# Optimization experiments

Hardware: AMD Instinct MI355X
Metric: run time of the kernel (lower is better)

Reference implementation:

```python
import jax, jax.numpy as jnp
from jax import lax
import numpy as np

WINDOW = 8
ENCOLEN = 128
HID = 128
INT_H = 128


def setup_inputs() -> dict:
    key = jax.random.key(0)
    ks = jax.random.split(key, 16)
    s = 0.05
    B, T = 512, 256
    return {
        "input_X": jax.random.normal(ks[0], (B, T, 7), jnp.float32),
        "W_ih": jax.random.normal(ks[1], (4 * HID, 5), jnp.float32) * s,
        "W_hh": jax.random.normal(ks[2], (4 * HID, HID), jnp.float32) * s,
        "b_ih": jax.random.normal(ks[3], (4 * HID,), jnp.float32) * s,
        "b_hh": jax.random.normal(ks[4], (4 * HID,), jnp.float32) * s,
        "fc1_w": jax.random.normal(ks[5], (HID, HID), jnp.float32) * s,
        "fc1_b": jax.random.normal(ks[6], (HID,), jnp.float32) * s,
        "fc2_w": jax.random.normal(ks[7], (1, HID), jnp.float32) * s,
        "fc2_b": jax.random.normal(ks[8], (1,), jnp.float32) * s,
        "int1_w": jax.random.normal(ks[9], (INT_H, 3), jnp.float32) * s,
        "int1_b": jax.random.normal(ks[10], (INT_H,), jnp.float32) * s,
        "int3_w": jax.random.normal(ks[11], (1, INT_H), jnp.float32) * s,
        "int3_b": jax.random.normal(ks[12], (1,), jnp.float32) * s,
        "scale_w": jax.random.normal(ks[13], (1, 1), jnp.float32) * s,
        "zone_w": jax.random.normal(ks[14], (1, 1), jnp.float32) * s,
    }


def _forward(input_X, W_ih, W_hh, b_ih, b_hh, fc1_w, fc1_b, fc2_w, fc2_b,
             int1_w, int1_b, int3_w, int3_b, scale_w, zone_w):
    B, T, _ = input_X.shape
    w = WINDOW
    T0 = input_X[:, :, 0:1]      # zone temperature
    Ext_X = input_X[:, :, 1:5]   # cols [1,2,3,4]
    Int_X = input_X[:, :, 3:6]   # cols [3,4,5]
    HVAC_X = input_X[:, :, 6:7]  # col [6]

    def lstm_chunk(h, c, xs):  # xs: [B, w, 5]
        def step(carry, x_t):
            h, c = carry
            g = x_t @ W_ih.T + b_ih + h @ W_hh.T + b_hh
            gi, gf, gg, go = jnp.split(g, 4, axis=-1)  # torch gate order i,f,g,o
            c = jax.nn.sigmoid(gf) * c + jax.nn.sigmoid(gi) * jnp.tanh(gg)
            h = jax.nn.sigmoid(go) * jnp.tanh(c)
            return (h, c), None
        (h, c), _ = lax.scan(step, (h, c), jnp.swapaxes(xs, 0, 1))
        return h, c  # final h == lstm_out[:, -1, :]

    def ext_module(h, c, xs):
        h, c = lstm_chunk(h, c, xs)
        o = jax.nn.relu(h @ fc1_w.T + fc1_b)
        return o @ fc2_w.T + fc2_b, h, c  # [B,1]

    # internal module is pointwise per timestep -> vectorize over all T
    # (note: FC2 in the torch module is defined but unused; faithful skip)
    int_all = jax.nn.sigmoid(
        jax.nn.relu(Int_X @ int1_w.T + int1_b) @ int3_w.T + int3_b
    ) @ scale_w.T  # [B,T,1]

    TOut = jnp.zeros((B, T, 1), input_X.dtype).at[:, :w].set(T0[:, :w])
    h = jnp.ones((B, HID), input_X.dtype)
    c = jnp.ones((B, HID), input_X.dtype)
    E = T0[:, w:w + 1, :]  # [B,1,1]

    def enc_step(carry, i):
        TOut, h, c, E = carry
        ratio = i.astype(input_X.dtype) / ENCOLEN
        TOut = lax.dynamic_update_slice(TOut, E, (0, i, 0))
        s = i - w + 1
        Tin = lax.dynamic_slice(T0, (0, s, 0), (B, w, 1))
        TOsl = lax.dynamic_slice(TOut, (0, s, 0), (B, w, 1))
        Exsl = lax.dynamic_slice(Ext_X, (0, s, 0), (B, w, 4))
        embed = jnp.concatenate([Tin * ratio + TOsl * (1.0 - ratio), Exsl], axis=2)
        ext, h, c = ext_module(h, c, embed)
        hv = lax.dynamic_slice(HVAC_X, (0, i, 0), (B, 1, 1))[:, 0]
        it = lax.dynamic_slice(int_all, (0, i, 0), (B, 1, 1))[:, 0]
        total = ext + hv + it  # [B,1]
        T0i = lax.dynamic_slice(T0, (0, i, 0), (B, 1, 1))
        E = ratio * T0i + (1.0 - ratio) * E + (total @ zone_w.T)[:, None, :]
        return (TOut, h, c, E), ext

    (TOut, h, c, E), ext_enc = lax.scan(enc_step, (TOut, h, c, E), jnp.arange(w, ENCOLEN))

    def dec_step(carry, i):
        TOut, h, c, E = carry
        TOut = lax.dynamic_update_slice(TOut, E, (0, i, 0))
        s = i - w + 1
        TOsl = lax.dynamic_slice(TOut, (0, s, 0), (B, w, 1))
        Exsl = lax.dynamic_slice(Ext_X, (0, s, 0), (B, w, 4))
        embed = jnp.concatenate([TOsl, Exsl], axis=2)
        ext, h, c = ext_module(h, c, embed)
        hv = lax.dynamic_slice(HVAC_X, (0, i, 0), (B, 1, 1))[:, 0]
        it = lax.dynamic_slice(int_all, (0, i, 0), (B, 1, 1))[:, 0]
        total = ext + hv + it
        E = (total @ zone_w.T)[:, None, :] + E
        return (TOut, h, c, E), ext

    (TOut, h, c, E), ext_dec = lax.scan(dec_step, (TOut, h, c, E), jnp.arange(ENCOLEN, T))

    Ext_list = jnp.zeros((B, T, 1), input_X.dtype)
    Ext_list = Ext_list.at[:, w:ENCOLEN].set(jnp.swapaxes(ext_enc, 0, 1))
    Ext_list = Ext_list.at[:, ENCOLEN:].set(jnp.swapaxes(ext_dec, 0, 1))
    Int_list = jnp.zeros((B, T, 1), input_X.dtype).at[:, w:].set(int_all[:, w:])
    HVAC_list = HVAC_X  # torch fills HVAC_list with HVAC_X at every step
    return TOut, HVAC_list, (Ext_list, Int_list)


def reference(input_X, W_ih, W_hh, b_ih, b_hh, fc1_w, fc1_b, fc2_w, fc2_b,
              int1_w, int1_b, int3_w, int3_b, scale_w, zone_w):
    return _forward(input_X, W_ih, W_hh, b_ih, b_hh, fc1_w, fc1_b, fc2_w, fc2_b,
                    int1_w, int1_b, int3_w, int3_b, scale_w, zone_w)
```

## Files before the change

kernel.cpp:

```cpp
#include <hip/hip_runtime.h>

#define BT   (512*256)
#define HB0  128
#define HB1  288
#define HLEN 448

using short8  = __attribute__((ext_vector_type(8))) short;
using floatx4 = __attribute__((ext_vector_type(4))) float;

__device__ inline unsigned short f2bf(float f){
  unsigned int u = __float_as_uint(f);
  u += 0x7FFFu + ((u >> 16) & 1u);
  return (unsigned short)(u >> 16);
}
__device__ inline float rcpf(float x){ return __builtin_amdgcn_rcpf(x); }

__global__ __launch_bounds__(256,1) void k_seq(
    const float* __restrict__ in,
    const float* __restrict__ Wih,  const float* __restrict__ Whh,
    const float* __restrict__ bih,  const float* __restrict__ bhh,
    const float* __restrict__ fc1w, const float* __restrict__ fc1b,
    const float* __restrict__ fc2w, const float* __restrict__ fc2b,
    const float* __restrict__ i1w,  const float* __restrict__ i1b,
    const float* __restrict__ i3w,  const float* __restrict__ i3b,
    const float* __restrict__ scw,  const float* __restrict__ zonew,
    float* __restrict__ out)
{
  __shared__ __align__(16) unsigned short hbuf[2][HLEN];
  __shared__ float xg[8192];
  __shared__ float obuf[256];
  __shared__ float toutl[512];
  __shared__ float inl[3584];
  __shared__ float itl[512];
  __shared__ float E_l[2], hvit[2], t0i[2];

  const int tid=threadIdx.x, wv=tid>>6, ln=tid&63, l15=ln&15, quad=ln>>4;
  const int bb=blockIdx.x;

  for(int p=tid;p<3584;p+=256) inl[p]=in[bb*3584+p];
  for(int p=tid;p<2*HLEN;p+=256) ((unsigned short*)hbuf)[p]=0;
  __syncthreads();
  hbuf[0][HB0 + (tid>>7)*(HB1-HB0) + (tid&127)] = 0x3F80;
  if(tid<16) toutl[(tid>>3)*256+(tid&7)] = inl[(tid>>3)*1792+(tid&7)*7];
  if(tid<2)  E_l[tid] = inl[tid*1792+56];

  {
    float* lw4 = xg;
    float* l3  = xg + 512;
    if(tid<128){
      lw4[tid*4+0]=i1w[tid*3+0]; lw4[tid*4+1]=i1w[tid*3+1];
      lw4[tid*4+2]=i1w[tid*3+2]; lw4[tid*4+3]=i1b[tid];
      l3[tid]=i3w[tid];
    }
    __syncthreads();
    const float b30=i3b[0], sc0=scw[0];
    #pragma unroll
    for(int rep=0;rep<2;rep++){
      int idx=tid+256*rep, b=idx>>8, t=idx&255;
      const float* row = inl + b*1792 + t*7;
      float x0=row[3],x1=row[4],x2=row[5], acc=0.f;
      #pragma unroll 8
      for(int j=0;j<128;j++){
        float r=fmaxf(lw4[j*4]*x0+lw4[j*4+1]*x1+lw4[j*4+2]*x2+lw4[j*4+3],0.f);
        acc += r*l3[j];
      }
      float v = rcpf(1.f+__expf(-(acc+b30)))*sc0;
      float itv = (t<8)?0.f:v;
      int gb = 2*bb+b;
      itl[b*256+t]=itv;
      out[3*BT+gb*256+t]=itv;
      out[BT+gb*256+t]=row[6];
      if(t<8){ out[gb*256+t]=row[0]; out[2*BT+gb*256+t]=0.f; }
    }
  }

  short8 wfr[4][2][4];
  short8 xfr[4][2];
  short8 ffr[2][4];
  float  bsum[4][2];
  #pragma unroll
  for(int g=0;g<4;g++){
    #pragma unroll
    for(int hh=0;hh<2;hh++){
      int n = 128*g + 32*wv + 16*hh + l15;
      bsum[g][hh] = bih[n]+bhh[n];
      #pragma unroll
      for(int Q=0;Q<4;Q++){
        short8 f;
        #pragma unroll
        for(int j=0;j<8;j++) f[j]=(short)f2bf(Whh[n*128 + Q*32 + quad*8 + j]);
        wfr[g][hh][Q]=f;
      }
      short8 f;
      #pragma unroll
      for(int j=0;j<8;j++){ int kk=quad*8+j; f[j]=(short)f2bf(kk<5?Wih[n*5+kk]:0.f); }
      xfr[g][hh]=f;
    }
  }
  #pragma unroll
  for(int hh=0;hh<2;hh++){
    int n = 32*wv + 16*hh + l15;
    #pragma unroll
    for(int Q=0;Q<4;Q++){
      short8 f;
      #pragma unroll
      for(int j=0;j<8;j++) f[j]=(short)f2bf(fc1w[n*128 + Q*32 + quad*8 + j]);
      ffr[hh][Q]=f;
    }
  }

  const int  u     = 32*wv + 16*(quad>>1) + l15;
  const int  bm    = quad & 1;
  const bool hi2   = quad >= 2;
  const int  aoff  = ((l15&3)==0) ? (HB0 + ((l15>>2)&1)*(HB1-HB0) + quad*8)
                                  : (quad*8);
  const int  xbase = bm*512 + u;
  const int  hwoff = HB0 + bm*(HB1-HB0) + u;
  const float fb    = fc1b[u];
  const float fw0   = fc2w[ln];
  const float fw1   = fc2w[64+ln];
  const float fc2b0 = fc2b[0];
  const float zw    = zonew[0];
  const floatx4 ZV  = {0.f,0.f,0.f,0.f};
  float c0 = 1.f;
  __syncthreads();

  #pragma unroll 1
  for(int i=8;i<256;i++){
    if(tid<2){
      float Ev=E_l[tid];
      toutl[tid*256+i]=Ev;
      out[(2*bb+tid)*256+i]=Ev;
      hvit[tid]=inl[tid*1792+i*7+6]+itl[tid*256+i];
      t0i[tid]=inl[tid*1792+i*7];
    }
    {
      short8 ea = 0;
      if(quad==0){
        int bE=l15>>3, kk=l15&7, p=i-7+kk;
        const float* rp = inl + bE*1792 + p*7;
        float tos = (p==i) ? E_l[bE] : toutl[bE*256+p];
        float tmix;
        if(i<128){
          float ratio=(float)i*0.0078125f;
          tmix = rp[0]*ratio + tos*(1.f-ratio);
        } else tmix = tos;
        ea[0]=(short)f2bf(tmix); ea[1]=(short)f2bf(rp[1]);
        ea[2]=(short)f2bf(rp[2]); ea[3]=(short)f2bf(rp[3]);
        ea[4]=(short)f2bf(rp[4]);
      }
      #pragma unroll
      for(int g=0;g<4;g++){
        #pragma unroll
        for(int hh=0;hh<2;hh++){
          floatx4 z=__builtin_amdgcn_mfma_f32_16x16x32_bf16(ea, xfr[g][hh], ZV,0,0,0);
          #pragma unroll
          for(int r=0;r<4;r++){
            int m=4*quad+r;
            xg[(m&7)*1024 + (m>>3)*512 + 128*g + 32*wv+16*hh+l15] = z[r]+bsum[g][hh];
          }
        }
      }
    }
    __syncthreads();

    #pragma unroll
    for(int k=0;k<8;k++){
      float xv0=xg[k*1024+xbase    ];
      float xv1=xg[k*1024+xbase+128];
      float xv2=xg[k*1024+xbase+256];
      float xv3=xg[k*1024+xbase+384];
      const unsigned short* ab = hbuf[k&1] + aoff;
      short8 a0=*(const short8*)(ab);
      short8 a1=*(const short8*)(ab+32);
      short8 a2=*(const short8*)(ab+64);
      short8 a3=*(const short8*)(ab+96);
      floatx4 acc[4][2];
      #pragma unroll
      for(int g=0;g<4;g++){
        #pragma unroll
        for(int hh=0;hh<2;hh++){
          floatx4 z=__builtin_amdgcn_mfma_f32_16x16x32_bf16(a0,wfr[g][hh][0],ZV,0,0,0);
          z=__builtin_amdgcn_mfma_f32_16x16x32_bf16(a1,wfr[g][hh][1],z,0,0,0);
          z=__builtin_amdgcn_mfma_f32_16x16x32_bf16(a2,wfr[g][hh][2],z,0,0,0);
          z=__builtin_amdgcn_mfma_f32_16x16x32_bf16(a3,wfr[g][hh][3],z,0,0,0);
          acc[g][hh]=z;
        }
      }
      float gi=(hi2?acc[0][1][0]:acc[0][0][0])+xv0;
      float gf=(hi2?acc[1][1][0]:acc[1][0][0])+xv1;
      float gg=(hi2?acc[2][1][0]:acc[2][0][0])+xv2;
      float go=(hi2?acc[3][1][0]:acc[3][0][0])+xv3;
      float ef =__expf(-gf);
      float egi=__expf(-gi);
      float egg=__expf(-2.f*gg);
      float sf = rcpf(1.f+ef);
      float itn=(1.f-egg)*rcpf((1.f+egi)*(1.f+egg));
      c0 = sf*c0 + itn;
      float ego=__expf(-go);
      float ec =__expf(-2.f*c0);
      float hv2=(1.f-ec)*rcpf((1.f+ego)*(1.f+ec));
      hbuf[(k+1)&1][hwoff]=f2bf(hv2);
      __syncthreads();
    }

    {
      const unsigned short* ab = hbuf[0] + aoff;
      short8 a0=*(const short8*)(ab);
      short8 a1=*(const short8*)(ab+32);
      short8 a2=*(const short8*)(ab+64);
      short8 a3=*(const short8*)(ab+96);
      floatx4 fa[2];
      #pragma unroll
      for(int hh=0;hh<2;hh++){
        floatx4 z=__builtin_amdgcn_mfma_f32_16x16x32_bf16(a0,ffr[hh][0],ZV,0,0,0);
        z=__builtin_amdgcn_mfma_f32_16x16x32_bf16(a1,ffr[hh][1],z,0,0,0);
        z=__builtin_amdgcn_mfma_f32_16x16x32_bf16(a2,ffr[hh][2],z,0,0,0);
        z=__builtin_amdgcn_mfma_f32_16x16x32_bf16(a3,ffr[hh][3],z,0,0,0);
        fa[hh]=z;
      }
      float fv = hi2 ? fa[1][0] : fa[0][0];
      obuf[bm*128+u]=fmaxf(fv+fb,0.f);
    }
    __syncthreads();

    if(wv<2){
      float v = obuf[wv*128+ln]*fw0 + obuf[wv*128+64+ln]*fw1;
      #pragma unroll
      for(int off=32; off; off>>=1) v += __shfl_xor(v, off, 64);
      if(ln==0){
        float ext = v + fc2b0;
        float total = ext + hvit[wv];
        float E = E_l[wv];
        if(i<128){
          float ratio=(float)i*0.0078125f;
          E = ratio*t0i[wv] + (1.f-ratio)*E + total*zw;
        } else {
          E = E + total*zw;
        }
        E_l[wv]=E;
        out[2*BT+(2*bb+wv)*256+i]=ext;
      }
    }
    __syncthreads();
  }
}

extern "C" void kernel_launch(void* const* d_in, const int* in_sizes, int n_in,
                              void* d_out, int out_size, void* d_ws, size_t ws_size,
                              hipStream_t stream)
{
  const float* in   = (const float*)d_in[0];
  const float* Wih  = (const float*)d_in[1];
  const float* Whh  = (const float*)d_in[2];
  const float* bih  = (const float*)d_in[3];
  const float* bhh  = (const float*)d_in[4];
  const float* fc1w = (const float*)d_in[5];
  const float* fc1b = (const float*)d_in[6];
  const float* fc2w = (const float*)d_in[7];
  const float* fc2b = (const float*)d_in[8];
  const float* i1w  = (const float*)d_in[9];
  const float* i1b  = (const float*)d_in[10];
  const float* i3w  = (const float*)d_in[11];
  const float* i3b  = (const float*)d_in[12];
  const float* scw  = (const float*)d_in[13];
  const float* zw   = (const float*)d_in[14];
  float* out = (float*)d_out;

  k_seq<<<dim3(256), dim3(256), 0, stream>>>(in, Wih, Whh, bih, bhh,
                                             fc1w, fc1b, fc2w, fc2b,
                                             i1w, i1b, i3w, i3b, scw, zw, out);
}
```

Baseline: 1.181 ms.

## Pack two independent batch groups per block with atomic-counter group barriers

Each 512-thread block now runs two independent 256-thread groups (128 blocks in total), and every __syncthreads is replaced by a per-group LDS atomic counter spin barrier. This lets the two groups' sequential LSTM steps interleave and hide each other's latency. To fit in LDS, the gate pre-activations, TOut and ext history, and ext features are stored as bf16. The ext and TOut outputs are buffered in LDS and written out once at the end. The trade-offs are lower precision for the stored values (TOut is rounded to bf16, which can drift through the recurrence) and spin-wait overhead from the software barriers.

```diff
diff --git a/kernel.cpp b/kernel.cpp
--- a/kernel.cpp
+++ b/kernel.cpp
@@ -4,6 +4,7 @@
 #define HB0  128
 #define HB1  288
 #define HLEN 448
+#define NG   2
 
 using short8  = __attribute__((ext_vector_type(8))) short;
 using floatx4 = __attribute__((ext_vector_type(4))) float;
@@ -13,9 +14,12 @@
   u += 0x7FFFu + ((u >> 16) & 1u);
   return (unsigned short)(u >> 16);
 }
+__device__ inline float bf2f(unsigned short u){
+  return __uint_as_float(((unsigned int)u) << 16);
+}
 __device__ inline float rcpf(float x){ return __builtin_amdgcn_rcpf(x); }
 
-__global__ __launch_bounds__(256,1) void k_seq(
+__global__ __launch_bounds__(512,2) void k_seq(
     const float* __restrict__ in,
     const float* __restrict__ Wih,  const float* __restrict__ Whh,
     const float* __restrict__ bih,  const float* __restrict__ bhh,
@@ -26,38 +30,52 @@
     const float* __restrict__ scw,  const float* __restrict__ zonew,
     float* __restrict__ out)
 {
-  __shared__ __align__(16) unsigned short hbuf[2][HLEN];
-  __shared__ float xg[8192];
-  __shared__ float obuf[256];
-  __shared__ float toutl[512];
-  __shared__ float inl[3584];
-  __shared__ float itl[512];
-  __shared__ float E_l[2], hvit[2], t0i[2];
-
-  const int tid=threadIdx.x, wv=tid>>6, ln=tid&63, l15=ln&15, quad=ln>>4;
-  const int bb=blockIdx.x;
-
-  for(int p=tid;p<3584;p+=256) inl[p]=in[bb*3584+p];
-  for(int p=tid;p<2*HLEN;p+=256) ((unsigned short*)hbuf)[p]=0;
+  __shared__ __align__(16) unsigned short hbuf[NG][2][HLEN];
+  __shared__ __align__(16) unsigned short xgu [NG][8192];
+  __shared__ __align__(8)  unsigned short toutl[NG][512];
+  __shared__ __align__(8)  unsigned short extl [NG][512];
+  __shared__ __align__(8)  unsigned short exl  [NG][2048];
+  __shared__ float t0l  [NG][512];
+  __shared__ float hvitl[NG][512];
+  __shared__ float obuf [NG][256];
+  __shared__ float E_l  [NG][2];
+  __shared__ unsigned int ctr[NG*16];
+
+  const int tid = threadIdx.x;
+  const int g   = tid >> 8;
+  const int t   = tid & 255;
+  const int wv  = t >> 6;
+  const int ln  = t & 63;
+  const int l15 = ln & 15;
+  const int quad= ln >> 4;
+  const int vbb = blockIdx.x*NG + g;
+
+  for(int p=t; p<512; p+=256){
+    int b=p>>8, tt=p&255;
+    const float* row = in + (2*vbb+b)*1792 + tt*7;
+    t0l[g][p] = row[0];
+    exl[g][p*4+0]=f2bf(row[1]); exl[g][p*4+1]=f2bf(row[2]);
+    exl[g][p*4+2]=f2bf(row[3]); exl[g][p*4+3]=f2bf(row[4]);
+  }
+  for(int p=t; p<2*HLEN; p+=256) ((unsigned short*)hbuf[g])[p]=0;
+  hbuf[g][0][HB0 + (t>>7)*(HB1-HB0) + (t&127)] = 0x3F80;
+  if(t<16) toutl[g][(t>>3)*256+(t&7)] = f2bf(in[(2*vbb+(t>>3))*1792+(t&7)*7]);
+  if(t<2)  E_l[g][t] = in[(2*vbb+t)*1792 + 56];
+  if(t==0) ctr[g*16]=0;
+  float* lw4 = (float*)&xgu[g][0];
+  float* l3  = lw4 + 512;
+  if(t<128){
+    lw4[t*4+0]=i1w[t*3+0]; lw4[t*4+1]=i1w[t*3+1];
+    lw4[t*4+2]=i1w[t*3+2]; lw4[t*4+3]=i1b[t];
+    l3[t]=i3w[t];
+  }
   __syncthreads();
-  hbuf[0][HB0 + (tid>>7)*(HB1-HB0) + (tid&127)] = 0x3F80;
-  if(tid<16) toutl[(tid>>3)*256+(tid&7)] = inl[(tid>>3)*1792+(tid&7)*7];
-  if(tid<2)  E_l[tid] = inl[tid*1792+56];
 
   {
-    float* lw4 = xg;
-    float* l3  = xg + 512;
-    if(tid<128){
-      lw4[tid*4+0]=i1w[tid*3+0]; lw4[tid*4+1]=i1w[tid*3+1];
-      lw4[tid*4+2]=i1w[tid*3+2]; lw4[tid*4+3]=i1b[tid];
-      l3[tid]=i3w[tid];
-    }
-    __syncthreads();
     const float b30=i3b[0], sc0=scw[0];
     #pragma unroll
-    for(int rep=0;rep<2;rep++){
-      int idx=tid+256*rep, b=idx>>8, t=idx&255;
-      const float* row = inl + b*1792 + t*7;
+    for(int b=0;b<2;b++){
+      const float* row = in + (2*vbb+b)*1792 + t*7;
       float x0=row[3],x1=row[4],x2=row[5], acc=0.f;
       #pragma unroll 8
       for(int j=0;j<128;j++){
@@ -66,8 +84,8 @@
       }
       float v = rcpf(1.f+__expf(-(acc+b30)))*sc0;
       float itv = (t<8)?0.f:v;
-      int gb = 2*bb+b;
-      itl[b*256+t]=itv;
+      int gb = 2*vbb+b;
+      hvitl[g][b*256+t] = row[6] + itv;
       out[3*BT+gb*256+t]=itv;
       out[BT+gb*256+t]=row[6];
       if(t<8){ out[gb*256+t]=row[0]; out[2*BT+gb*256+t]=0.f; }
@@ -79,22 +97,22 @@
   short8 ffr[2][4];
   float  bsum[4][2];
   #pragma unroll
-  for(int g=0;g<4;g++){
+  for(int gg=0;gg<4;gg++){
     #pragma unroll
     for(int hh=0;hh<2;hh++){
-      int n = 128*g + 32*wv + 16*hh + l15;
-      bsum[g][hh] = bih[n]+bhh[n];
+      int n = 128*gg + 32*wv + 16*hh + l15;
+      bsum[gg][hh] = bih[n]+bhh[n];
       #pragma unroll
       for(int Q=0;Q<4;Q++){
         short8 f;
         #pragma unroll
         for(int j=0;j<8;j++) f[j]=(short)f2bf(Whh[n*128 + Q*32 + quad*8 + j]);
-        wfr[g][hh][Q]=f;
+        wfr[gg][hh][Q]=f;
       }
       short8 f;
       #pragma unroll
       for(int j=0;j<8;j++){ int kk=quad*8+j; f[j]=(short)f2bf(kk<5?Wih[n*5+kk]:0.f); }
-      xfr[g][hh]=f;
+      xfr[gg][hh]=f;
     }
   }
   #pragma unroll
@@ -123,89 +141,92 @@
   const float zw    = zonew[0];
   const floatx4 ZV  = {0.f,0.f,0.f,0.f};
   float c0 = 1.f;
-  __syncthreads();
+
+  unsigned int tgt = 0;
+  volatile unsigned int* vct = (volatile unsigned int*)&ctr[g*16];
+  #define GSYNC() do{ tgt += 4; __threadfence_block();                    \
+      if(ln==0) atomicAdd((unsigned int*)&ctr[g*16], 1u);                 \
+      while(*vct < tgt){}                                                 \
+      __threadfence_block(); }while(0)
+
+  GSYNC();
 
   #pragma unroll 1
   for(int i=8;i<256;i++){
-    if(tid<2){
-      float Ev=E_l[tid];
-      toutl[tid*256+i]=Ev;
-      out[(2*bb+tid)*256+i]=Ev;
-      hvit[tid]=inl[tid*1792+i*7+6]+itl[tid*256+i];
-      t0i[tid]=inl[tid*1792+i*7];
-    }
+    if(t<2) toutl[g][t*256+i] = f2bf(E_l[g][t]);
     {
       short8 ea = 0;
       if(quad==0){
         int bE=l15>>3, kk=l15&7, p=i-7+kk;
-        const float* rp = inl + bE*1792 + p*7;
-        float tos = (p==i) ? E_l[bE] : toutl[bE*256+p];
+        float t0v = t0l[g][bE*256+p];
+        float tos = (p==i) ? E_l[g][bE] : bf2f(toutl[g][bE*256+p]);
         float tmix;
         if(i<128){
           float ratio=(float)i*0.0078125f;
-          tmix = rp[0]*ratio + tos*(1.f-ratio);
+          tmix = t0v*ratio + tos*(1.f-ratio);
         } else tmix = tos;
-        ea[0]=(short)f2bf(tmix); ea[1]=(short)f2bf(rp[1]);
-        ea[2]=(short)f2bf(rp[2]); ea[3]=(short)f2bf(rp[3]);
-        ea[4]=(short)f2bf(rp[4]);
-      }
-      #pragma unroll
-      for(int g=0;g<4;g++){
+        ea[0]=(short)f2bf(tmix);
+        ea[1]=(short)exl[g][(bE*256+p)*4+0]; ea[2]=(short)exl[g][(bE*256+p)*4+1];
+        ea[3]=(short)exl[g][(bE*256+p)*4+2]; ea[4]=(short)exl[g][(bE*256+p)*4+3];
+      }
+      #pragma unroll
+      for(int gg=0;gg<4;gg++){
         #pragma unroll
         for(int hh=0;hh<2;hh++){
-          floatx4 z=__builtin_amdgcn_mfma_f32_16x16x32_bf16(ea, xfr[g][hh], ZV,0,0,0);
+          floatx4 z=__builtin_amdgcn_mfma_f32_16x16x32_bf16(ea, xfr[gg][hh], ZV,0,0,0);
           #pragma unroll
           for(int r=0;r<4;r++){
             int m=4*quad+r;
-            xg[(m&7)*1024 + (m>>3)*512 + 128*g + 32*wv+16*hh+l15] = z[r]+bsum[g][hh];
+            xgu[g][(m&7)*1024 + (m>>3)*512 + 128*gg + 32*wv+16*hh+l15]
+              = f2bf(z[r]+bsum[gg][hh]);
           }
         }
       }
     }
-    __syncthreads();
+    GSYNC();
 
     #pragma unroll
     for(int k=0;k<8;k++){
-      float xv0=xg[k*1024+xbase    ];
-      float xv1=xg[k*1024+xbase+128];
-      float xv2=xg[k*1024+xbase+256];
-      float xv3=xg[k*1024+xbase+384];
-      const unsigned short* ab = hbuf[k&1] + aoff;
+      float xv0=bf2f(xgu[g][k*1024+xbase    ]);
+      float xv1=bf2f(xgu[g][k*1024+xbase+128]);
+      float xv2=bf2f(xgu[g][k*1024+xbase+256]);
+      float xv3=bf2f(xgu[g][k*1024+xbase+384]);
+      const unsigned short* ab = &hbuf[g][k&1][0] + aoff;
       short8 a0=*(const short8*)(ab);
       short8 a1=*(const short8*)(ab+32);
       short8 a2=*(const short8*)(ab+64);
       short8 a3=*(const short8*)(ab+96);
       floatx4 acc[4][2];
       #pragma unroll
-      for(int g=0;g<4;g++){
+      for(int gg=0;gg<4;gg++){
         #pragma unroll
         for(int hh=0;hh<2;hh++){
-          floatx4 z=__builtin_amdgcn_mfma_f32_16x16x32_bf16(a0,wfr[g][hh][0],ZV,0,0,0);
-          z=__builtin_amdgcn_mfma_f32_16x16x32_bf16(a1,wfr[g][hh][1],z,0,0,0);
-          z=__builtin_amdgcn_mfma_f32_16x16x32_bf16(a2,wfr[g][hh][2],z,0,0,0);
-          z=__builtin_amdgcn_mfma_f32_16x16x32_bf16(a3,wfr[g][hh][3],z,0,0,0);
-          acc[g][hh]=z;
+          floatx4 z=__builtin_amdgcn_mfma_f32_16x16x32_bf16(a0,wfr[gg][hh][0],ZV,0,0,0);
+          z=__builtin_amdgcn_mfma_f32_16x16x32_bf16(a1,wfr[gg][hh][1],z,0,0,0);
+          z=__builtin_amdgcn_mfma_f32_16x16x32_bf16(a2,wfr[gg][hh][2],z,0,0,0);
+          z=__builtin_amdgcn_mfma_f32_16x16x32_bf16(a3,wfr[gg][hh][3],z,0,0,0);
+          acc[gg][hh]=z;
         }
       }
       float gi=(hi2?acc[0][1][0]:acc[0][0][0])+xv0;
       float gf=(hi2?acc[1][1][0]:acc[1][0][0])+xv1;
-      float gg=(hi2?acc[2][1][0]:acc[2][0][0])+xv2;
+      float gg2=(hi2?acc[2][1][0]:acc[2][0][0])+xv2;
       float go=(hi2?acc[3][1][0]:acc[3][0][0])+xv3;
       float ef =__expf(-gf);
       float egi=__expf(-gi);
-      float egg=__expf(-2.f*gg);
+      float egg=__expf(-2.f*gg2);
       float sf = rcpf(1.f+ef);
       float itn=(1.f-egg)*rcpf((1.f+egi)*(1.f+egg));
       c0 = sf*c0 + itn;
       float ego=__expf(-go);
       float ec =__expf(-2.f*c0);
       float hv2=(1.f-ec)*rcpf((1.f+ego)*(1.f+ec));
-      hbuf[(k+1)&1][hwoff]=f2bf(hv2);
-      __syncthreads();
+      hbuf[g][(k+1)&1][hwoff]=f2bf(hv2);
+      GSYNC();
     }
 
     {
-      const unsigned short* ab = hbuf[0] + aoff;
+      const unsigned short* ab = &hbuf[g][0][0] + aoff;
       short8 a0=*(const short8*)(ab);
       short8 a1=*(const short8*)(ab+32);
       short8 a2=*(const short8*)(ab+64);
@@ -220,30 +241,39 @@
         fa[hh]=z;
       }
       float fv = hi2 ? fa[1][0] : fa[0][0];
-      obuf[bm*128+u]=fmaxf(fv+fb,0.f);
-    }
-    __syncthreads();
+      obuf[g][bm*128+u]=fmaxf(fv+fb,0.f);
+    }
+    GSYNC();
 
     if(wv<2){
-      float v = obuf[wv*128+ln]*fw0 + obuf[wv*128+64+ln]*fw1;
+      float v = obuf[g][wv*128+ln]*fw0 + obuf[g][wv*128+64+ln]*fw1;
       #pragma unroll
       for(int off=32; off; off>>=1) v += __shfl_xor(v, off, 64);
       if(ln==0){
-        float ext = v + fc2b0;
-        float total = ext + hvit[wv];
-        float E = E_l[wv];
+        float ext   = v + fc2b0;
+        float total = ext + hvitl[g][wv*256+i];
+        float E = E_l[g][wv];
         if(i<128){
           float ratio=(float)i*0.0078125f;
-          E = ratio*t0i[wv] + (1.f-ratio)*E + total*zw;
+          E = ratio*t0l[g][wv*256+i] + (1.f-ratio)*E + total*zw;
         } else {
           E = E + total*zw;
         }
-        E_l[wv]=E;
-        out[2*BT+(2*bb+wv)*256+i]=ext;
-      }
-    }
-    __syncthreads();
-  }
+        E_l[g][wv]=E;
+        extl[g][wv*256+i]=f2bf(ext);
+      }
+    }
+    GSYNC();
+  }
+
+  for(int p=t; p<496; p+=256){
+    int b = (p>=248) ? 1 : 0;
+    int i2 = p - b*248 + 8;
+    int gb = 2*vbb + b;
+    out[gb*256+i2]        = bf2f(toutl[g][b*256+i2]);
+    out[2*BT+gb*256+i2]   = bf2f(extl[g][b*256+i2]);
+  }
+  #undef GSYNC
 }
 
 extern "C" void kernel_launch(void* const* d_in, const int* in_sizes, int n_in,
@@ -267,7 +297,7 @@
   const float* zw   = (const float*)d_in[14];
   float* out = (float*)d_out;
 
-  k_seq<<<dim3(256), dim3(256), 0, stream>>>(in, Wih, Whh, bih, bhh,
+  k_seq<<<dim3(128), dim3(512), 0, stream>>>(in, Wih, Whh, bih, bhh,
                                              fc1w, fc1b, fc2w, fc2b,
                                              i1w, i1b, i3w, i3b, scw, zw, out);
 }
```

Measured after the change: 1.842 ms. +56.0%, slower.

## Double block to 512 threads, halve per-wave MFMA work, bf16 LDS staging

Applied to the files above, without the earlier changes.

Each block now runs 512 threads (8 waves), so each wave owns 16 hidden units instead of 32 and issues half as many MFMA chains per recurrent step. Gate pre-activations, external inputs and output history move to bf16 in LDS. The fc2 reduction is done with per-wave shuffles plus a small partial-sum array, and every thread tracks E redundantly. The T and ext outputs are buffered in LDS and written once at the end. The aim is to shorten the serial per-step critical path, at the cost of heavier barriers across 8 waves and extra rounding error: T is stored as bf16 before output and fed back into the recurrence, and the ext output is also rounded to bf16.

```diff
diff --git a/kernel.cpp b/kernel.cpp
--- a/kernel.cpp
+++ b/kernel.cpp
@@ -13,9 +13,12 @@
   u += 0x7FFFu + ((u >> 16) & 1u);
   return (unsigned short)(u >> 16);
 }
+__device__ inline float bf2f(unsigned short u){
+  return __uint_as_float(((unsigned int)u) << 16);
+}
 __device__ inline float rcpf(float x){ return __builtin_amdgcn_rcpf(x); }
 
-__global__ __launch_bounds__(256,1) void k_seq(
+__global__ __launch_bounds__(512,1) void k_seq(
     const float* __restrict__ in,
     const float* __restrict__ Wih,  const float* __restrict__ Whh,
     const float* __restrict__ bih,  const float* __restrict__ bhh,
@@ -27,138 +30,131 @@
     float* __restrict__ out)
 {
   __shared__ __align__(16) unsigned short hbuf[2][HLEN];
-  __shared__ float xg[8192];
-  __shared__ float obuf[256];
-  __shared__ float toutl[512];
-  __shared__ float inl[3584];
-  __shared__ float itl[512];
-  __shared__ float E_l[2], hvit[2], t0i[2];
-
-  const int tid=threadIdx.x, wv=tid>>6, ln=tid&63, l15=ln&15, quad=ln>>4;
-  const int bb=blockIdx.x;
-
-  for(int p=tid;p<3584;p+=256) inl[p]=in[bb*3584+p];
-  for(int p=tid;p<2*HLEN;p+=256) ((unsigned short*)hbuf)[p]=0;
+  __shared__ __align__(16) unsigned short xg[8192];
+  __shared__ __align__(8)  unsigned short toutl[512];
+  __shared__ __align__(8)  unsigned short extl[512];
+  __shared__ __align__(16) unsigned short exl[2048];
+  __shared__ float t0l[512];
+  __shared__ float hvitl[512];
+  __shared__ float parts[16];
+
+  const int tid = threadIdx.x;
+  const int wv  = tid >> 6;
+  const int ln  = tid & 63;
+  const int l15 = ln & 15;
+  const int quad= ln >> 4;
+  const int bb  = blockIdx.x;
+
+  {
+    int b=tid>>8, tt=tid&255;
+    const float* row = in + (2*bb+b)*1792 + tt*7;
+    t0l[tid] = row[0];
+    exl[tid*4+0]=f2bf(row[1]); exl[tid*4+1]=f2bf(row[2]);
+    exl[tid*4+2]=f2bf(row[3]); exl[tid*4+3]=f2bf(row[4]);
+  }
+  for(int p=tid; p<2*HLEN; p+=512) ((unsigned short*)hbuf)[p]=0;
+  if(tid<16) toutl[(tid>>3)*256+(tid&7)] = f2bf(in[(2*bb+(tid>>3))*1792+(tid&7)*7]);
+  float* lw4 = (float*)&xg[0];
+  float* l3  = lw4 + 512;
+  if(tid<128){
+    lw4[tid*4+0]=i1w[tid*3+0]; lw4[tid*4+1]=i1w[tid*3+1];
+    lw4[tid*4+2]=i1w[tid*3+2]; lw4[tid*4+3]=i1b[tid];
+    l3[tid]=i3w[tid];
+  }
   __syncthreads();
-  hbuf[0][HB0 + (tid>>7)*(HB1-HB0) + (tid&127)] = 0x3F80;
-  if(tid<16) toutl[(tid>>3)*256+(tid&7)] = inl[(tid>>3)*1792+(tid&7)*7];
-  if(tid<2)  E_l[tid] = inl[tid*1792+56];
+  if(tid<256) hbuf[0][HB0 + (tid>>7)*(HB1-HB0) + (tid&127)] = 0x3F80;
 
   {
-    float* lw4 = xg;
-    float* l3  = xg + 512;
-    if(tid<128){
-      lw4[tid*4+0]=i1w[tid*3+0]; lw4[tid*4+1]=i1w[tid*3+1];
-      lw4[tid*4+2]=i1w[tid*3+2]; lw4[tid*4+3]=i1b[tid];
-      l3[tid]=i3w[tid];
-    }
-    __syncthreads();
     const float b30=i3b[0], sc0=scw[0];
-    #pragma unroll
-    for(int rep=0;rep<2;rep++){
-      int idx=tid+256*rep, b=idx>>8, t=idx&255;
-      const float* row = inl + b*1792 + t*7;
-      float x0=row[3],x1=row[4],x2=row[5], acc=0.f;
-      #pragma unroll 8
-      for(int j=0;j<128;j++){
-        float r=fmaxf(lw4[j*4]*x0+lw4[j*4+1]*x1+lw4[j*4+2]*x2+lw4[j*4+3],0.f);
-        acc += r*l3[j];
-      }
-      float v = rcpf(1.f+__expf(-(acc+b30)))*sc0;
-      float itv = (t<8)?0.f:v;
-      int gb = 2*bb+b;
-      itl[b*256+t]=itv;
-      out[3*BT+gb*256+t]=itv;
-      out[BT+gb*256+t]=row[6];
-      if(t<8){ out[gb*256+t]=row[0]; out[2*BT+gb*256+t]=0.f; }
-    }
-  }
-
-  short8 wfr[4][2][4];
-  short8 xfr[4][2];
-  short8 ffr[2][4];
-  float  bsum[4][2];
+    int b=tid>>8, t=tid&255;
+    const float* row = in + (2*bb+b)*1792 + t*7;
+    float x0=row[3],x1=row[4],x2=row[5], acc=0.f;
+    #pragma unroll 8
+    for(int j=0;j<128;j++){
+      float r=fmaxf(lw4[j*4]*x0+lw4[j*4+1]*x1+lw4[j*4+2]*x2+lw4[j*4+3],0.f);
+      acc += r*l3[j];
+    }
+    float v = rcpf(1.f+__expf(-(acc+b30)))*sc0;
+    float itv = (t<8)?0.f:v;
+    int gb = 2*bb+b;
+    hvitl[tid] = row[6] + itv;
+    out[3*BT+gb*256+t]=itv;
+    out[BT+gb*256+t]=row[6];
+    if(t<8){ out[gb*256+t]=row[0]; out[2*BT+gb*256+t]=0.f; }
+  }
+
+  short8 wfr[4][4];
+  short8 xfr[4];
+  short8 ffr[4];
+  float  bsum[4];
   #pragma unroll
   for(int g=0;g<4;g++){
-    #pragma unroll
-    for(int hh=0;hh<2;hh++){
-      int n = 128*g + 32*wv + 16*hh + l15;
-      bsum[g][hh] = bih[n]+bhh[n];
-      #pragma unroll
-      for(int Q=0;Q<4;Q++){
-        short8 f;
-        #pragma unroll
-        for(int j=0;j<8;j++) f[j]=(short)f2bf(Whh[n*128 + Q*32 + quad*8 + j]);
-        wfr[g][hh][Q]=f;
-      }
-      short8 f;
-      #pragma unroll
-      for(int j=0;j<8;j++){ int kk=quad*8+j; f[j]=(short)f2bf(kk<5?Wih[n*5+kk]:0.f); }
-      xfr[g][hh]=f;
-    }
-  }
-  #pragma unroll
-  for(int hh=0;hh<2;hh++){
-    int n = 32*wv + 16*hh + l15;
+    int n = 128*g + 16*wv + l15;
+    bsum[g] = bih[n]+bhh[n];
     #pragma unroll
     for(int Q=0;Q<4;Q++){
       short8 f;
       #pragma unroll
-      for(int j=0;j<8;j++) f[j]=(short)f2bf(fc1w[n*128 + Q*32 + quad*8 + j]);
-      ffr[hh][Q]=f;
-    }
-  }
-
-  const int  u     = 32*wv + 16*(quad>>1) + l15;
+      for(int j=0;j<8;j++) f[j]=(short)f2bf(Whh[n*128 + Q*32 + quad*8 + j]);
+      wfr[g][Q]=f;
+    }
+    short8 f;
+    #pragma unroll
+    for(int j=0;j<8;j++){ int kk=quad*8+j; f[j]=(short)f2bf(kk<5?Wih[n*5+kk]:0.f); }
+    xfr[g]=f;
+  }
+  {
+    int n2 = 16*wv + l15;
+    #pragma unroll
+    for(int Q=0;Q<4;Q++){
+      short8 f;
+      #pragma unroll
+      for(int j=0;j<8;j++) f[j]=(short)f2bf(fc1w[n2*128 + Q*32 + quad*8 + j]);
+      ffr[Q]=f;
+    }
+  }
+
+  const int  u     = 16*wv + l15;
   const int  bm    = quad & 1;
-  const bool hi2   = quad >= 2;
   const int  aoff  = ((l15&3)==0) ? (HB0 + ((l15>>2)&1)*(HB1-HB0) + quad*8)
                                   : (quad*8);
   const int  xbase = bm*512 + u;
   const int  hwoff = HB0 + bm*(HB1-HB0) + u;
   const float fb    = fc1b[u];
-  const float fw0   = fc2w[ln];
-  const float fw1   = fc2w[64+ln];
+  const float fcw_u = fc2w[u];
   const float fc2b0 = fc2b[0];
-  const float zw    = zonew[0];
+  const float zwv   = zonew[0];
   const floatx4 ZV  = {0.f,0.f,0.f,0.f};
+  const short8  Z8  = 0;
+  float E0 = in[(2*bb)*1792 + 56];
+  float E1 = in[(2*bb+1)*1792 + 56];
   float c0 = 1.f;
+  if(tid==0){ toutl[8]=f2bf(E0); toutl[256+8]=f2bf(E1); }
   __syncthreads();
 
   #pragma unroll 1
   for(int i=8;i<256;i++){
-    if(tid<2){
-      float Ev=E_l[tid];
-      toutl[tid*256+i]=Ev;
-      out[(2*bb+tid)*256+i]=Ev;
-      hvit[tid]=inl[tid*1792+i*7+6]+itl[tid*256+i];
-      t0i[tid]=inl[tid*1792+i*7];
-    }
     {
-      short8 ea = 0;
+      short8 ea = Z8;
       if(quad==0){
         int bE=l15>>3, kk=l15&7, p=i-7+kk;
-        const float* rp = inl + bE*1792 + p*7;
-        float tos = (p==i) ? E_l[bE] : toutl[bE*256+p];
+        float tos = bf2f(toutl[bE*256+p]);
         float tmix;
         if(i<128){
           float ratio=(float)i*0.0078125f;
-          tmix = rp[0]*ratio + tos*(1.f-ratio);
+          tmix = t0l[bE*256+p]*ratio + tos*(1.f-ratio);
         } else tmix = tos;
-        ea[0]=(short)f2bf(tmix); ea[1]=(short)f2bf(rp[1]);
-        ea[2]=(short)f2bf(rp[2]); ea[3]=(short)f2bf(rp[3]);
-        ea[4]=(short)f2bf(rp[4]);
+        ea[0]=(short)f2bf(tmix);
+        ea[1]=(short)exl[(bE*256+p)*4+0]; ea[2]=(short)exl[(bE*256+p)*4+1];
+        ea[3]=(short)exl[(bE*256+p)*4+2]; ea[4]=(short)exl[(bE*256+p)*4+3];
       }
       #pragma unroll
       for(int g=0;g<4;g++){
+        floatx4 z=__builtin_amdgcn_mfma_f32_16x16x32_bf16(ea, xfr[g], ZV,0,0,0);
         #pragma unroll
-        for(int hh=0;hh<2;hh++){
-          floatx4 z=__builtin_amdgcn_mfma_f32_16x16x32_bf16(ea, xfr[g][hh], ZV,0,0,0);
-          #pragma unroll
-          for(int r=0;r<4;r++){
-            int m=4*quad+r;
-            xg[(m&7)*1024 + (m>>3)*512 + 128*g + 32*wv+16*hh+l15] = z[r]+bsum[g][hh];
-          }
+        for(int r=0;r<4;r++){
+          int m=4*quad+r;
+          xg[(m&7)*1024 + (m>>3)*512 + 128*g + u] = f2bf(z[r]+bsum[g]);
         }
       }
     }
@@ -166,31 +162,28 @@
 
     #pragma unroll
     for(int k=0;k<8;k++){
-      float xv0=xg[k*1024+xbase    ];
-      float xv1=xg[k*1024+xbase+128];
-      float xv2=xg[k*1024+xbase+256];
-      float xv3=xg[k*1024+xbase+384];
-      const unsigned short* ab = hbuf[k&1] + aoff;
+      float xv0=bf2f(xg[k*1024+xbase    ]);
+      float xv1=bf2f(xg[k*1024+xbase+128]);
+      float xv2=bf2f(xg[k*1024+xbase+256]);
+      float xv3=bf2f(xg[k*1024+xbase+384]);
+      const unsigned short* ab = &hbuf[k&1][0] + aoff;
       short8 a0=*(const short8*)(ab);
       short8 a1=*(const short8*)(ab+32);
       short8 a2=*(const short8*)(ab+64);
       short8 a3=*(const short8*)(ab+96);
-      floatx4 acc[4][2];
+      floatx4 acc[4];
       #pragma unroll
       for(int g=0;g<4;g++){
-        #pragma unroll
-        for(int hh=0;hh<2;hh++){
-          floatx4 z=__builtin_amdgcn_mfma_f32_16x16x32_bf16(a0,wfr[g][hh][0],ZV,0,0,0);
-          z=__builtin_amdgcn_mfma_f32_16x16x32_bf16(a1,wfr[g][hh][1],z,0,0,0);
-          z=__builtin_amdgcn_mfma_f32_16x16x32_bf16(a2,wfr[g][hh][2],z,0,0,0);
-          z=__builtin_amdgcn_mfma_f32_16x16x32_bf16(a3,wfr[g][hh][3],z,0,0,0);
-          acc[g][hh]=z;
-        }
-      }
-      float gi=(hi2?acc[0][1][0]:acc[0][0][0])+xv0;
-      float gf=(hi2?acc[1][1][0]:acc[1][0][0])+xv1;
-      float gg=(hi2?acc[2][1][0]:acc[2][0][0])+xv2;
-      float go=(hi2?acc[3][1][0]:acc[3][0][0])+xv3;
+        floatx4 z=__builtin_amdgcn_mfma_f32_16x16x32_bf16(a0,wfr[g][0],ZV,0,0,0);
+        z=__builtin_amdgcn_mfma_f32_16x16x32_bf16(a1,wfr[g][1],z,0,0,0);
+        z=__builtin_amdgcn_mfma_f32_16x16x32_bf16(a2,wfr[g][2],z,0,0,0);
+        z=__builtin_amdgcn_mfma_f32_16x16x32_bf16(a3,wfr[g][3],z,0,0,0);
+        acc[g]=z;
+      }
+      float gi=acc[0][0]+xv0;
+      float gf=acc[1][0]+xv1;
+      float gg=acc[2][0]+xv2;
+      float go=acc[3][0]+xv3;
       float ef =__expf(-gf);
       float egi=__expf(-gi);
       float egg=__expf(-2.f*gg);
@@ -200,49 +193,65 @@
       float ego=__expf(-go);
       float ec =__expf(-2.f*c0);
       float hv2=(1.f-ec)*rcpf((1.f+ego)*(1.f+ec));
-      hbuf[(k+1)&1][hwoff]=f2bf(hv2);
+      hbuf[(k+1)&1][hwoff] = f2bf(hv2);
       __syncthreads();
     }
 
     {
-      const unsigned short* ab = hbuf[0] + aoff;
+      const unsigned short* ab = &hbuf[0][0] + aoff;
       short8 a0=*(const short8*)(ab);
       short8 a1=*(const short8*)(ab+32);
       short8 a2=*(const short8*)(ab+64);
       short8 a3=*(const short8*)(ab+96);
-      floatx4 fa[2];
-      #pragma unroll
-      for(int hh=0;hh<2;hh++){
-        floatx4 z=__builtin_amdgcn_mfma_f32_16x16x32_bf16(a0,ffr[hh][0],ZV,0,0,0);
-        z=__builtin_amdgcn_mfma_f32_16x16x32_bf16(a1,ffr[hh][1],z,0,0,0);
-        z=__builtin_amdgcn_mfma_f32_16x16x32_bf16(a2,ffr[hh][2],z,0,0,0);
-        z=__builtin_amdgcn_mfma_f32_16x16x32_bf16(a3,ffr[hh][3],z,0,0,0);
-        fa[hh]=z;
-      }
-      float fv = hi2 ? fa[1][0] : fa[0][0];
-      obuf[bm*128+u]=fmaxf(fv+fb,0.f);
+      floatx4 z=__builtin_amdgcn_mfma_f32_16x16x32_bf16(a0,ffr[0],ZV,0,0,0);
+      z=__builtin_amdgcn_mfma_f32_16x16x32_bf16(a1,ffr[1],z,0,0,0);
+      z=__builtin_amdgcn_mfma_f32_16x16x32_bf16(a2,ffr[2],z,0,0,0);
+      z=__builtin_amdgcn_mfma_f32_16x16x32_bf16(a3,ffr[3],z,0,0,0);
+      float pv = fmaxf(z[0]+fb,0.f)*fcw_u;
+      float v0 = (quad==0) ? pv : 0.f;
+      float v1 = (quad==1) ? pv : 0.f;
+      #pragma unroll
+      for(int off=32; off; off>>=1){
+        v0 += __shfl_xor(v0, off, 64);
+        v1 += __shfl_xor(v1, off, 64);
+      }
+      if(ln==0){ parts[wv*2]=v0; parts[wv*2+1]=v1; }
     }
     __syncthreads();
 
-    if(wv<2){
-      float v = obuf[wv*128+ln]*fw0 + obuf[wv*128+64+ln]*fw1;
-      #pragma unroll
-      for(int off=32; off; off>>=1) v += __shfl_xor(v, off, 64);
-      if(ln==0){
-        float ext = v + fc2b0;
-        float total = ext + hvit[wv];
-        float E = E_l[wv];
-        if(i<128){
-          float ratio=(float)i*0.0078125f;
-          E = ratio*t0i[wv] + (1.f-ratio)*E + total*zw;
-        } else {
-          E = E + total*zw;
+    {
+      float ext0 = parts[0]+parts[2]+parts[4]+parts[6]
+                 + parts[8]+parts[10]+parts[12]+parts[14] + fc2b0;
+      float ext1 = parts[1]+parts[3]+parts[5]+parts[7]
+                 + parts[9]+parts[11]+parts[13]+parts[15] + fc2b0;
+      float tot0 = ext0 + hvitl[i];
+      float tot1 = ext1 + hvitl[256+i];
+      if(i<128){
+        float ratio=(float)i*0.0078125f;
+        E0 = ratio*t0l[i]     + (1.f-ratio)*E0 + tot0*zwv;
+        E1 = ratio*t0l[256+i] + (1.f-ratio)*E1 + tot1*zwv;
+      } else {
+        E0 += tot0*zwv;
+        E1 += tot1*zwv;
+      }
+      if(tid==0){
+        extl[i]     = f2bf(ext0);
+        extl[256+i] = f2bf(ext1);
+        if(i<255){
+          toutl[i+1]     = f2bf(E0);
+          toutl[257+i]   = f2bf(E1);
         }
-        E_l[wv]=E;
-        out[2*BT+(2*bb+wv)*256+i]=ext;
       }
     }
     __syncthreads();
+  }
+
+  for(int p=tid; p<496; p+=512){
+    int b = (p>=248) ? 1 : 0;
+    int i2 = p - b*248 + 8;
+    int gb = 2*bb + b;
+    out[gb*256+i2]      = bf2f(toutl[b*256+i2]);
+    out[2*BT+gb*256+i2] = bf2f(extl[b*256+i2]);
   }
 }
 
@@ -267,7 +276,7 @@
   const float* zw   = (const float*)d_in[14];
   float* out = (float*)d_out;
 
-  k_seq<<<dim3(256), dim3(256), 0, stream>>>(in, Wih, Whh, bih, bhh,
+  k_seq<<<dim3(256), dim3(512), 0, stream>>>(in, Wih, Whh, bih, bhh,
                                              fc1w, fc1b, fc2w, fc2b,
                                              i1w, i1b, i3w, i3b, scw, zw, out);
 }
```

New measurement: 1.228 ms. +4.0%, slower.
